# Performance work log

Measured on AMD Instinct MI355X. Metric: run time of the kernel, lower is better.

The kernel has to match this reference:

```python
import jax, jax.numpy as jnp
import numpy as np

M = 64; N_SC = 32; SPS = 8; LENCP = 16; NUMOFDM = 256 // N_SC
BETA = 0.5; SPAN = 16; LENRRC = SPAN * SPS + 1  # 129
FC = 25e6; FS = 10e6 * SPS
CLIP = 1.2; SNR = 10.0; THRES = 8.0
LEN_T = NUMOFDM * (M + LENCP)              # 640
NUMSAMPLES = LEN_T * SPS + LENRRC * 2      # 5378
L1 = LEN_T * SPS + LENRRC - 1              # 5248 (post pulse-shaping length)


def make_rrc():
    # standard root-raised-cosine, unit energy
    t = np.arange(-SPAN * SPS // 2, SPAN * SPS // 2 + 1) / SPS
    h = np.zeros_like(t)
    eps = 1e-9
    t0 = np.abs(t) < eps
    ts = np.abs(np.abs(t) - 1.0 / (4 * BETA)) < eps
    reg = ~(t0 | ts)
    tr = t[reg]
    h[reg] = (np.sin(np.pi * tr * (1 - BETA)) + 4 * BETA * tr * np.cos(np.pi * tr * (1 + BETA))) / (
        np.pi * tr * (1 - (4 * BETA * tr) ** 2))
    h[t0] = 1 + BETA * (4 / np.pi - 1)
    h[ts] = (BETA / np.sqrt(2)) * ((1 + 2 / np.pi) * np.sin(np.pi / (4 * BETA)) +
                                   (1 - 2 / np.pi) * np.cos(np.pi / (4 * BETA)))
    h = h / np.sqrt(np.sum(h ** 2))
    return h.astype(np.float32)


def _conv_full(u, k):
    # torch F.conv1d(x, k.flip(), padding=K-1) == full convolution with k
    K = k.shape[0]
    return jax.lax.conv_general_dilated(
        u[:, None, :], k[::-1][None, None, :], (1,), [(K - 1, K - 1)],
        dimension_numbers=('NCH', 'OIH', 'NCH'))[:, 0, :]


def _pulse_filter(c, rrc):
    return _conv_full(c.real, rrc) + 1j * _conv_full(c.imag, rrc)


def _power_norm(z):
    m = jnp.mean(z, axis=1, keepdims=True)
    s = jnp.std(z, axis=1, ddof=1, keepdims=True)  # torch.std is unbiased
    return (z - m) / (s + 1e-8)


def _forward(x, W_enc, b_enc, W_dec, b_dec, rrc, awgn, startloc):
    B = x.shape[0]
    # --- encoder (linear proxy for ResNetTx) -> 512 reals ---
    z = x.reshape(B, -1) @ W_enc + b_enc
    z = _power_norm(z)
    c = z.reshape(B, 256, 2)
    c = (c[..., 0] + 1j * c[..., 1]).reshape(B, NUMOFDM, N_SC)  # complex64
    # --- DFT precoding ---
    c = jnp.fft.fftshift(jnp.fft.fft(c, axis=-1, norm='ortho'), axes=-1)
    # --- subcarrier mapping (contiguous block, mapping==1) ---
    loc = jnp.arange(startloc, startloc + N_SC)
    data_f = jnp.zeros((B, NUMOFDM, M), jnp.complex64).at[:, :, loc].set(c)
    data_t = jnp.fft.ifft(data_f, axis=-1, norm='ortho')
    data_t = jnp.concatenate([data_t[:, :, -LENCP:], data_t], axis=-1)  # CP
    data_t = data_t.reshape(B, LEN_T)
    # --- zero-stuffed upsampling + RRC pulse shaping ---
    over = jnp.zeros((B, LEN_T * SPS), jnp.complex64).at[:, ::SPS].set(data_t)
    xc = _pulse_filter(over, rrc)  # (B, L1)
    # --- carrier mixing ---
    n = jnp.arange(NUMSAMPLES, dtype=jnp.float32)
    cos_c = jnp.sqrt(2.0) * jnp.cos(2 * jnp.pi * FC * n / FS)
    sin_c = jnp.sqrt(2.0) * jnp.sin(2 * jnp.pi * FC * n / FS)
    data_x = xc.real * cos_c[:L1] - xc.imag * sin_c[:L1]
    # --- clipping ---
    thr = CLIP * jnp.sqrt(jnp.mean(jnp.square(data_x), axis=1, keepdims=True))
    over_amp = jax.nn.relu(jnp.abs(data_x) - thr)
    data_x = (1.0 - over_amp / (jnp.abs(data_x) + 1e-8)) * data_x
    # --- PAPR ---
    tstart = (LENRRC + 1) // 2
    p = jnp.square(data_x[:, tstart:tstart + LEN_T * SPS])
    PAPRdB = 10.0 * jnp.log10(jnp.max(p, axis=1) / jnp.mean(p, axis=1))
    PAPRloss = jnp.mean(jax.nn.relu(PAPRdB - THRES))
    # --- AWGN channel (no fading) ---
    data_r = data_x + awgn
    # --- downconversion + matched filter ---
    rc = data_r * cos_c[:L1] - 1j * (data_r * sin_c[:L1])
    filt = _pulse_filter(rc, rrc)  # (B, L1 + LENRRC - 1) = (B, 5376)
    y = filt[:, LENRRC - 1:filt.shape[1] - LENRRC:SPS]  # (B, LEN_T)
    y = y.reshape(B, NUMOFDM, M + LENCP)[:, :, LENCP:]
    y = jnp.fft.fft(y, axis=-1, norm='ortho')[:, :, loc]
    y = jnp.fft.ifft(jnp.fft.fftshift(y, axes=-1), axis=-1, norm='ortho')
    y = y.reshape(B, NUMOFDM * N_SC)
    y = jnp.stack([y.real, y.imag], axis=-1).reshape(B, 8, 8, 8)
    # --- decoder (linear proxy for ResNetRx) ---
    out = (y.reshape(B, 512) @ W_dec + b_dec).reshape(B, 3, 32, 32)
    return out, PAPRdB, PAPRloss


def setup_inputs() -> dict:
    key = jax.random.key(0)
    ks = jax.random.split(key, 4)
    B = 1024
    x = jax.random.normal(ks[0], (B, 3, 32, 32), jnp.float32)
    W_enc = jax.random.normal(ks[1], (3072, 512), jnp.float32) * 0.02
    b_enc = jnp.zeros((512,), jnp.float32)
    W_dec = jax.random.normal(ks[2], (512, 3072), jnp.float32) * 0.05
    b_dec = jnp.zeros((3072,), jnp.float32)
    rrc = jnp.asarray(make_rrc())
    noise_std = 10.0 ** (-SNR / 20.0)
    awgn = jax.random.normal(ks[3], (B, L1), jnp.float32) * noise_std
    return {"x": x, "W_enc": W_enc, "b_enc": b_enc, "W_dec": W_dec,
            "b_dec": b_dec, "rrc": rrc, "awgn": awgn, "startloc": 7}


def reference(x, W_enc, b_enc, W_dec, b_dec, rrc, awgn, startloc):
    return _forward(x, W_enc, b_enc, W_dec, b_dec, rrc, awgn, startloc)
```

## Files before the change

kernel.cpp:

```cpp
#include <hip/hip_runtime.h>
#include <hip/hip_bf16.h>
#include <math.h>

#define L1_     5248
#define LENRRC_ 129
#define TSTART_ 65
#define NWIN_   5120
#define SWZ(m) ((m) + ((m) >> 3))

typedef __attribute__((ext_vector_type(8))) short s16x8;
typedef __attribute__((ext_vector_type(4))) float f32x4;

__device__ inline ushort bf16_rne(float x) {
    unsigned xb = __float_as_uint(x);
    return (ushort)((xb + 0x7fffu + ((xb >> 16) & 1u)) >> 16);
}

__device__ inline float wave_sum(float v) {
    #pragma unroll
    for (int m = 32; m > 0; m >>= 1) v += __shfl_xor(v, m, 64);
    return v;
}
__device__ inline float wave_max(float v) {
    #pragma unroll
    for (int m = 32; m > 0; m >>= 1) v = fmaxf(v, __shfl_xor(v, m, 64));
    return v;
}

__device__ inline void gl_lds16(const void* g, void* l) {
    __builtin_amdgcn_global_load_lds(
        (const __attribute__((address_space(1))) unsigned int*)g,
        (__attribute__((address_space(3))) unsigned int*)l, 16, 0, 0);
}

__global__ __launch_bounds__(256) void pack_k(const float* __restrict__ W1,
        const float* __restrict__ W2, const float* __restrict__ benc,
        ushort* __restrict__ w1t, ushort* __restrict__ w2t, float* __restrict__ z)
{
    __shared__ ushort tile[64][70];
    const int blk = blockIdx.x, tid = threadIdx.x;
    if (blk < 768) {
        const float* W; ushort* T; int K, N, n0, k0;
        if (blk < 384) {
            int idx = blk;
            W = W1; T = w1t; K = 3072; N = 512;
            n0 = (idx & 7) * 64; k0 = (idx >> 3) * 64;
        } else {
            int idx = blk - 384;
            W = W2; T = w2t; K = 512; N = 3072;
            n0 = (idx % 48) * 64; k0 = (idx / 48) * 64;
        }
        const int cr = tid >> 4, cc = (tid & 15) * 4;
        #pragma unroll
        for (int i = 0; i < 4; ++i) {
            int kk = i * 16 + cr;
            float4 v = *(const float4*)&W[(size_t)(k0 + kk) * N + n0 + cc];
            tile[kk][cc]     = bf16_rne(v.x);
            tile[kk][cc + 1] = bf16_rne(v.y);
            tile[kk][cc + 2] = bf16_rne(v.z);
            tile[kk][cc + 3] = bf16_rne(v.w);
        }
        __syncthreads();
        #pragma unroll
        for (int i = 0; i < 4; ++i) {
            int nn = i * 16 + cr;
            ushort4 h;
            h.x = tile[cc][nn]; h.y = tile[cc + 1][nn];
            h.z = tile[cc + 2][nn]; h.w = tile[cc + 3][nn];
            *(ushort4*)&T[(size_t)(n0 + nn) * K + k0 + cc] = h;
        }
    } else {
        int i = (blk - 768) * 256 + tid;
        z[i] = benc[i & 511];
    }
}

__global__ __launch_bounds__(256) void gemm1_k(const float* __restrict__ Ax,
        const ushort* __restrict__ Bb, float* __restrict__ C, int M, int N, int K,
        int partial)
{
    __shared__ __attribute__((aligned(16))) ushort Asl[64 * 64];
    __shared__ __attribute__((aligned(16))) ushort Bsl[128 * 64];
    const int tid = threadIdx.x;
    const int lane = tid & 63, wave = tid >> 6;
    const int wm = (wave >> 1) * 32, wn = (wave & 1) * 64;
    const int m0 = blockIdx.y * 64, n0 = blockIdx.x * 128;
    const int kch = K / 8, kbeg = blockIdx.z * kch, kend = kbeg + kch;
    const int fm = lane & 15, q = lane >> 4;
    f32x4 acc[2][4] = {};

    int arow[2], akb[2], brow[4], bkb[4];
    #pragma unroll
    for (int j = 0; j < 2; ++j) {
        int c = ((wave * 2 + j) << 6) + lane;
        arow[j] = c >> 3; akb[j] = (c & 7) ^ (arow[j] & 7);
    }
    #pragma unroll
    for (int j = 0; j < 4; ++j) {
        int c = ((wave * 4 + j) << 6) + lane;
        brow[j] = c >> 3; bkb[j] = (c & 7) ^ (brow[j] & 7);
    }

    for (int kt = kbeg; kt < kend; kt += 64) {
        #pragma unroll
        for (int j = 0; j < 4; ++j)
            gl_lds16(&Bb[(size_t)(n0 + brow[j]) * K + kt + bkb[j] * 8],
                     &Bsl[(wave * 4 + j) << 9]);
        #pragma unroll
        for (int j = 0; j < 2; ++j) {
            int c = ((wave * 2 + j) << 6) + lane;
            const float* src = &Ax[(size_t)(m0 + arow[j]) * K + kt + akb[j] * 8];
            float4 v0 = *(const float4*)src;
            float4 v1 = *(const float4*)(src + 4);
            s16x8 hv;
            hv[0] = (short)bf16_rne(v0.x); hv[1] = (short)bf16_rne(v0.y);
            hv[2] = (short)bf16_rne(v0.z); hv[3] = (short)bf16_rne(v0.w);
            hv[4] = (short)bf16_rne(v1.x); hv[5] = (short)bf16_rne(v1.y);
            hv[6] = (short)bf16_rne(v1.z); hv[7] = (short)bf16_rne(v1.w);
            *(s16x8*)&Asl[c * 8] = hv;
        }
        __syncthreads();
        #pragma unroll
        for (int ks = 0; ks < 2; ++ks) {
            s16x8 a[2], b[4];
            #pragma unroll
            for (int mf = 0; mf < 2; ++mf) {
                int r = wm + mf * 16 + fm;
                a[mf] = *(const s16x8*)&Asl[(r << 6) + ((((ks << 2) + q) ^ (r & 7)) << 3)];
            }
            #pragma unroll
            for (int nf = 0; nf < 4; ++nf) {
                int r = wn + nf * 16 + fm;
                b[nf] = *(const s16x8*)&Bsl[(r << 6) + ((((ks << 2) + q) ^ (r & 7)) << 3)];
            }
            #pragma unroll
            for (int mf = 0; mf < 2; ++mf)
                #pragma unroll
                for (int nf = 0; nf < 4; ++nf)
                    acc[mf][nf] = __builtin_amdgcn_mfma_f32_16x16x32_bf16(a[mf], b[nf], acc[mf][nf], 0, 0, 0);
        }
        __syncthreads();
    }

    if (partial) {
        float* Cs = C + (size_t)blockIdx.z * ((size_t)M * N);
        #pragma unroll
        for (int mf = 0; mf < 2; ++mf)
            #pragma unroll
            for (int nf = 0; nf < 4; ++nf)
                #pragma unroll
                for (int r = 0; r < 4; ++r) {
                    int m = m0 + wm + mf * 16 + q * 4 + r;
                    int n = n0 + wn + nf * 16 + fm;
                    Cs[(size_t)m * N + n] = acc[mf][nf][r];
                }
    } else {
        #pragma unroll
        for (int mf = 0; mf < 2; ++mf)
            #pragma unroll
            for (int nf = 0; nf < 4; ++nf)
                #pragma unroll
                for (int r = 0; r < 4; ++r) {
                    int m = m0 + wm + mf * 16 + q * 4 + r;
                    int n = n0 + wn + nf * 16 + fm;
                    atomicAdd(&C[(size_t)m * N + n], acc[mf][nf][r]);
                }
    }
}

__global__ __launch_bounds__(256) void gemm2_k(const ushort* __restrict__ Ab,
        const ushort* __restrict__ Bb, const float* __restrict__ bias,
        const float* __restrict__ papr, float* __restrict__ C,
        float* __restrict__ out_loss, int M, int N, int K)
{
    __shared__ __attribute__((aligned(16))) ushort Asl[64 * 64];
    __shared__ __attribute__((aligned(16))) ushort Bsl[64 * 64];
    __shared__ float red[4];
    const int tid = threadIdx.x;
    const int lane = tid & 63, wave = tid >> 6;
    const int wm = (wave >> 1) * 32, wn = (wave & 1) * 32;
    const int m0 = blockIdx.y * 64, n0 = blockIdx.x * 64;
    const int fm = lane & 15, q = lane >> 4;
    f32x4 acc[2][2] = {};

    int srow[2], skb[2];
    #pragma unroll
    for (int j = 0; j < 2; ++j) {
        int c = ((wave * 2 + j) << 6) + lane;
        srow[j] = c >> 3; skb[j] = (c & 7) ^ (srow[j] & 7);
    }

    for (int kt = 0; kt < K; kt += 64) {
        #pragma unroll
        for (int j = 0; j < 2; ++j) {
            gl_lds16(&Ab[(size_t)(m0 + srow[j]) * K + kt + skb[j] * 8],
                     &Asl[(wave * 2 + j) << 9]);
            gl_lds16(&Bb[(size_t)(n0 + srow[j]) * K + kt + skb[j] * 8],
                     &Bsl[(wave * 2 + j) << 9]);
        }
        __syncthreads();
        #pragma unroll
        for (int ks = 0; ks < 2; ++ks) {
            s16x8 a[2], b[2];
            #pragma unroll
            for (int mf = 0; mf < 2; ++mf) {
                int r = wm + mf * 16 + fm;
                a[mf] = *(const s16x8*)&Asl[(r << 6) + ((((ks << 2) + q) ^ (r & 7)) << 3)];
            }
            #pragma unroll
            for (int nf = 0; nf < 2; ++nf) {
                int r = wn + nf * 16 + fm;
                b[nf] = *(const s16x8*)&Bsl[(r << 6) + ((((ks << 2) + q) ^ (r & 7)) << 3)];
            }
            #pragma unroll
            for (int mf = 0; mf < 2; ++mf)
                #pragma unroll
                for (int nf = 0; nf < 2; ++nf)
                    acc[mf][nf] = __builtin_amdgcn_mfma_f32_16x16x32_bf16(a[mf], b[nf], acc[mf][nf], 0, 0, 0);
        }
        __syncthreads();
    }

    #pragma unroll
    for (int mf = 0; mf < 2; ++mf)
        #pragma unroll
        for (int nf = 0; nf < 2; ++nf)
            #pragma unroll
            for (int r = 0; r < 4; ++r) {
                int m = m0 + wm + mf * 16 + q * 4 + r;
                int n = n0 + wn + nf * 16 + fm;
                C[(size_t)m * N + n] = acc[mf][nf][r] + bias[n];
            }

    if (blockIdx.x == 0 && blockIdx.y == 0) {
        float s = 0.f;
        for (int i = tid; i < 1024; i += 256) { float v = papr[i] - 8.f; s += v > 0.f ? v : 0.f; }
        s = wave_sum(s);
        if (lane == 0) red[wave] = s;
        __syncthreads();
        if (tid == 0) *out_loss = (red[0] + red[1] + red[2] + red[3]) * (1.f / 1024.f);
    }
}

__global__ __launch_bounds__(512, 4) void mega_k(const float* __restrict__ z,
        const float* __restrict__ benc,
        const float* __restrict__ rrc, const float* __restrict__ awgn,
        const int* __restrict__ slocp, ushort* __restrict__ y5b,
        float* __restrict__ papr, float* __restrict__ out_papr, int nsp)
{
    __shared__ float  zl[2][512];
    __shared__ float2 trti[2][672];
    __shared__ float  hl[132];
    __shared__ float  csl[16], ssl[16];
    __shared__ float2 cs64[64];
    __shared__ float  ct[64];
    __shared__ __attribute__((aligned(16))) float2 gcs[130];
    __shared__ float  dxr[2][SWZ(L1_ - 1) + 1];
    __shared__ float  red[2][8], red2[2][8];

    const int b0 = blockIdx.x * 2, b1 = b0 + 1;
    const int tid = threadIdx.x;
    const int lane = tid & 63, wv = tid >> 6;
    const int sloc = *slocp;
    const float S2048 = 0.02209708691207961f;

    if (tid < 64) {
        float ang = 0.09817477042468103f * (float)tid;
        float s, c; sincosf(ang, &s, &c);
        cs64[tid] = make_float2(c, s);
    }
    if (tid >= 64 && tid < 80) {
        int t = tid - 64;
        float ang = 1.9634954084936207f * (float)t;
        float s, c; sincosf(ang, &s, &c);
        csl[t] = 1.4142135623730951f * c; ssl[t] = 1.4142135623730951f * s;
    }
    if (tid >= 96 && tid < 160) {
        int t = (tid - 96) & 31, row = (tid - 96) >> 5;
        int idx = (t < 16) ? t : (640 + t);
        trti[row][idx] = make_float2(0.f, 0.f);
    }
    if (tid >= 160 && tid < 224) {
        int j = tid - 160;
        float v = 0.f;
        if (j & 1) { float s, c; sincosf(0.04908738521234052f * (float)j, &s, &c); v = c / s; }
        ct[j] = v;
    }
    if (tid >= 256 && tid < 256 + LENRRC_) hl[tid - 256] = rrc[tid - 256];

    float va, vb;
    if (nsp) {
        va = benc[tid]; vb = va;
        const float* zp0 = z + (size_t)b0 * 512;
        const float* zp1 = z + (size_t)b1 * 512;
        for (int s = 0; s < nsp; ++s) {
            va += zp0[(size_t)s * 524288 + tid];
            vb += zp1[(size_t)s * 524288 + tid];
        }
    } else {
        va = z[(size_t)b0 * 512 + tid];
        vb = z[(size_t)b1 * 512 + tid];
    }
    __syncthreads();

    if (tid < LENRRC_) {
        int neg = (16 - (tid & 15)) & 15;
        gcs[tid] = make_float2(hl[tid] * csl[neg], hl[tid] * ssl[neg]);
    }

    {
        float S0 = wave_sum(va), Q0 = wave_sum(va * va);
        float S1 = wave_sum(vb), Q1 = wave_sum(vb * vb);
        if (lane == 0) { red[0][wv] = S0; red2[0][wv] = Q0; red[1][wv] = S1; red2[1][wv] = Q1; }
    }
    __syncthreads();
    {
        float S0 = 0.f, Q0 = 0.f, S1 = 0.f, Q1 = 0.f;
        #pragma unroll
        for (int w = 0; w < 8; ++w) {
            S0 += red[0][w]; Q0 += red2[0][w];
            S1 += red[1][w]; Q1 += red2[1][w];
        }
        float m0 = S0 * (1.f / 512.f), m1 = S1 * (1.f / 512.f);
        float i0 = 1.f / (sqrtf((Q0 - S0 * m0) * (1.f / 511.f)) + 1e-8f);
        float i1 = 1.f / (sqrtf((Q1 - S1 * m1) * (1.f / 511.f)) + 1e-8f);
        float sg = ((tid >> 1) & 1) ? -1.f : 1.f;
        zl[0][tid] = (va - m0) * i0 * sg;
        zl[1][tid] = (vb - m1) * i1 * sg;
    }
    __syncthreads();

    {
        int r = tid >> 8, t = tid & 255;
        int s = t >> 5, j = t & 31;
        int base = s * 80;
        const float2* zs = (const float2*)&zl[r][s * 64];
        int n = 2 * j + 1;
        float Zr = 0.f, Zi = 0.f, Tr = 0.f, Ti = 0.f;
        #pragma unroll 4
        for (int q = 0; q < 32; ++q) {
            float2 a = zs[q];
            float w = ct[(n - 2 * q) & 63];
            Zr += a.x; Zi += a.y;
            Tr += a.x * w; Ti += a.y * w;
        }
        {
            float2 cw = cs64[(n * sloc) & 63];
            float Ar = Zr - Ti, Ai = Zi + Tr;
            float dr = S2048 * (Ar * cw.x - Ai * cw.y);
            float di = S2048 * (Ai * cw.x + Ar * cw.y);
            trti[r][base + 32 + n] = make_float2(dr, di);
            if (n >= 48) trti[r][base + n - 32] = make_float2(dr, di);
        }
        {
            int n2 = 2 * j;
            float2 a = zs[j];
            float2 cw = cs64[(n2 * sloc) & 63];
            const float RS2 = 0.7071067811865476f;
            float dr = RS2 * (a.x * cw.x - a.y * cw.y);
            float di = RS2 * (a.y * cw.x + a.x * cw.y);
            trti[r][base + 32 + n2] = make_float2(dr, di);
            if (n2 >= 48) trti[r][base + n2 - 32] = make_float2(dr, di);
        }
    }
    __syncthreads();

    float ss0 = 0.f, ss1 = 0.f;
    for (int tsk = tid; tsk < 1312; tsk += 512) {
        int a = tsk >> 1, g = tsk & 1;
        float ar0[4] = {}, ai0[4] = {}, ar1[4] = {}, ai1[4] = {};
        #pragma unroll 4
        for (int d = 0; d < 16; ++d) {
            float2 t0 = trti[0][16 + a - d];
            float2 t1 = trti[1][16 + a - d];
            #pragma unroll
            for (int r = 0; r < 4; ++r) {
                float h = hl[g * 4 + r + 8 * d];
                ar0[r] += t0.x * h; ai0[r] += t0.y * h;
                ar1[r] += t1.x * h; ai1[r] += t1.y * h;
            }
        }
        if (g == 0) {
            float2 t0 = trti[0][a], t1 = trti[1][a];
            float h = hl[128];
            ar0[0] += t0.x * h; ai0[0] += t0.y * h;
            ar1[0] += t1.x * h; ai1[0] += t1.y * h;
        }
        int cb = (a & 1) * 8;
        #pragma unroll
        for (int r = 0; r < 4; ++r) {
            int rr = g * 4 + r;
            float cv = csl[cb + rr], sv = ssl[cb + rr];
            float v0 = ar0[r] * cv - ai0[r] * sv;
            float v1 = ar1[r] * cv - ai1[r] * sv;
            dxr[0][SWZ(a * 8 + rr)] = v0;
            dxr[1][SWZ(a * 8 + rr)] = v1;
            ss0 += v0 * v0; ss1 += v1 * v1;
        }
    }
    ss0 = wave_sum(ss0); ss1 = wave_sum(ss1);
    if (lane == 0) { red[0][wv] = ss0; red[1][wv] = ss1; }
    __syncthreads();
    float thr0, thr1;
    {
        float S0 = 0.f, S1 = 0.f;
        #pragma unroll
        for (int w = 0; w < 8; ++w) { S0 += red[0][w]; S1 += red[1][w]; }
        thr0 = 1.2f * sqrtf(S0 / (float)L1_);
        thr1 = 1.2f * sqrtf(S1 / (float)L1_);
    }
    __syncthreads();

    float pm0 = 0.f, ps0 = 0.f, pm1 = 0.f, ps1 = 0.f;
    {
        const float4* ag0 = (const float4*)&awgn[(size_t)b0 * L1_];
        const float4* ag1 = (const float4*)&awgn[(size_t)b1 * L1_];
        for (int ii = tid; ii < 1312; ii += 512) {
            float4 a0 = ag0[ii], a1 = ag1[ii];
            int i = ii * 4;
            #pragma unroll
            for (int e = 0; e < 4; ++e) {
                int idx = i + e;
                bool win = (idx >= TSTART_ && idx < TSTART_ + NWIN_);
                float aw0 = (e == 0) ? a0.x : (e == 1) ? a0.y : (e == 2) ? a0.z : a0.w;
                float aw1 = (e == 0) ? a1.x : (e == 1) ? a1.y : (e == 2) ? a1.z : a1.w;
                {
                    float x = dxr[0][SWZ(idx)];
                    float ax = fabsf(x);
                    float over = fmaxf(ax - thr0, 0.f);
                    float y = (1.f - over / (ax + 1e-8f)) * x;
                    if (win) { float p = y * y; ps0 += p; pm0 = fmaxf(pm0, p); }
                    dxr[0][SWZ(idx)] = y + aw0;
                }
                {
                    float x = dxr[1][SWZ(idx)];
                    float ax = fabsf(x);
                    float over = fmaxf(ax - thr1, 0.f);
                    float y = (1.f - over / (ax + 1e-8f)) * x;
                    if (win) { float p = y * y; ps1 += p; pm1 = fmaxf(pm1, p); }
                    dxr[1][SWZ(idx)] = y + aw1;
                }
            }
        }
    }
    ps0 = wave_sum(ps0); pm0 = wave_max(pm0);
    ps1 = wave_sum(ps1); pm1 = wave_max(pm1);
    if (lane == 0) { red[0][wv] = ps0; red2[0][wv] = pm0; red[1][wv] = ps1; red2[1][wv] = pm1; }
    __syncthreads();
    if (tid == 0) {
        float s0 = 0.f, m0 = 0.f, s1 = 0.f, m1 = 0.f;
        #pragma unroll
        for (int w = 0; w < 8; ++w) {
            s0 += red[0][w]; m0 = fmaxf(m0, red2[0][w]);
            s1 += red[1][w]; m1 = fmaxf(m1, red2[1][w]);
        }
        float p0 = 10.f * log10f(m0 / (s0 / (float)NWIN_));
        float p1 = 10.f * log10f(m1 / (s1 / (float)NWIN_));
        papr[b0] = p0; out_papr[b0] = p0;
        papr[b1] = p1; out_papr[b1] = p1;
    }
    __syncthreads();

    {
        int s = wv, n = lane;
        int T0 = s * 80 + n + 32;
        int base = 9 * T0;
        float ar0 = 0.f, ai0 = 0.f, ar1 = 0.f, ai1 = 0.f;
        int db = 0;
        #pragma unroll 4
        for (int e = 0; e < 16; ++e) {
            float4 g01 = *(const float4*)&gcs[db];
            float4 g23 = *(const float4*)&gcs[db + 2];
            float4 g45 = *(const float4*)&gcs[db + 4];
            float4 g67 = *(const float4*)&gcs[db + 6];
            float gx[8] = { g01.x, g01.z, g23.x, g23.z, g45.x, g45.z, g67.x, g67.z };
            float gy[8] = { g01.y, g01.w, g23.y, g23.w, g45.y, g45.w, g67.y, g67.w };
            #pragma unroll
            for (int u = 0; u < 8; ++u) {
                int off = (u == 0) ? 0 : (u + 1);
                float v0 = dxr[0][base - off];
                float v1 = dxr[1][base - off];
                ar0 += v0 * gx[u]; ai0 += v0 * gy[u];
                ar1 += v1 * gx[u]; ai1 += v1 * gy[u];
            }
            base -= 9; db += 8;
        }
        {
            float2 g = gcs[128];
            float v0 = dxr[0][base], v1 = dxr[1][base];
            ar0 += v0 * g.x; ai0 += v0 * g.y;
            ar1 += v1 * g.x; ai1 += v1 * g.y;
        }
        bool odd = (n & 1);
        float wr0 = odd ? -ar0 : ar0, wi0 = odd ? ai0 : -ai0;
        float wr1 = odd ? -ar1 : ar1, wi1 = odd ? ai1 : -ai1;
        float2 cw = cs64[(n * sloc) & 63];
        trti[0][s * 64 + n] = make_float2(wr0 * cw.x + wi0 * cw.y, wi0 * cw.x - wr0 * cw.y);
        trti[1][s * 64 + n] = make_float2(wr1 * cw.x + wi1 * cw.y, wi1 * cw.x - wr1 * cw.y);
    }
    __syncthreads();

    {
        int r = tid >> 8, t = tid & 255;
        int s = t >> 5, q = t & 31;
        const float2* wt = &trti[r][s * 64];
        float Wr = 0.f, Wi = 0.f, Ur = 0.f, Ui = 0.f;
        #pragma unroll 4
        for (int u = 0; u < 32; ++u) {
            float2 a = wt[2 * u + 1];
            float w = ct[(2 * q - 2 * u - 1) & 63];
            Wr += a.x; Wi += a.y;
            Ur += a.x * w; Ui += a.y * w;
        }
        float2 e = wt[2 * q];
        float sgn = (q & 1) ? -S2048 : S2048;
        float yr = sgn * (32.f * e.x + Wr - Ui);
        float yi = sgn * (32.f * e.y + Wi + Ur);
        ushort2 h; h.x = bf16_rne(yr); h.y = bf16_rne(yi);
        *(ushort2*)&y5b[(size_t)(b0 + r) * 512 + (s * 32 + q) * 2] = h;
    }
}

extern "C" void kernel_launch(void* const* d_in, const int* in_sizes, int n_in,
                              void* d_out, int out_size, void* d_ws, size_t ws_size,
                              hipStream_t stream) {
    const float* x    = (const float*)d_in[0];
    const float* Wenc = (const float*)d_in[1];
    const float* benc = (const float*)d_in[2];
    const float* Wdec = (const float*)d_in[3];
    const float* bdec = (const float*)d_in[4];
    const float* rrc  = (const float*)d_in[5];
    const float* awgn = (const float*)d_in[6];
    const int* sloc   = (const int*)d_in[7];
    float* out = (float*)d_out;

    char* wsb = (char*)d_ws;
    ushort* w1t  = (ushort*)wsb;                     wsb += (size_t)512 * 3072 * 2;
    ushort* w2t  = (ushort*)wsb;                     wsb += (size_t)3072 * 512 * 2;
    ushort* y5b  = (ushort*)wsb;                     wsb += (size_t)1024 * 512 * 2;
    float*  papr = (float*)wsb;                      wsb += 1024 * 4;
    float*  zbuf = (float*)wsb;
    size_t head = (size_t)((char*)zbuf - (char*)d_ws);
    int partial = (ws_size >= head + (size_t)8 * 1024 * 512 * 4) ? 1 : 0;

    float* out_papr = out + (size_t)1024 * 3072;
    float* out_loss = out_papr + 1024;

    pack_k<<<partial ? 768 : 2816, 256, 0, stream>>>(Wenc, Wdec, benc, w1t, w2t, zbuf);
    gemm1_k<<<dim3(4, 16, 8), 256, 0, stream>>>(x, w1t, zbuf, 1024, 512, 3072, partial);
    mega_k<<<512, 512, 0, stream>>>(zbuf, benc, rrc, awgn, sloc, y5b, papr, out_papr,
                                    partial ? 8 : 0);
    gemm2_k<<<dim3(48, 16, 1), 256, 0, stream>>>(y5b, w2t, bdec, papr, out, out_loss, 1024, 3072, 512);
}
```

Measured before the change: 145.2 us.

## Double mega_k block size to 1024 threads and split per-row work

Launches the fused OFDM kernel with 1024 threads per block instead of 512. Normalization, the final receive filter and the DFT stages now give each thread one batch row, or half of a DFT sum combined with a lane shuffle, instead of two rows or the full sum. The goal is more in-flight threads and shorter per-thread dependency chains on a latency-bound kernel. The costs are heavier register pressure under the 1024-thread launch bound, idle threads in loops that only cover 1312 tasks, and extra shuffles and barrier cost.

After: 153.8 us. +6.0%, slower.

```diff
diff --git a/kernel.cpp b/kernel.cpp
--- a/kernel.cpp
+++ b/kernel.cpp
@@ -242,7 +242,7 @@
     }
 }
 
-__global__ __launch_bounds__(512, 4) void mega_k(const float* __restrict__ z,
+__global__ __launch_bounds__(1024, 4) void mega_k(const float* __restrict__ z,
         const float* __restrict__ benc,
         const float* __restrict__ rrc, const float* __restrict__ awgn,
         const int* __restrict__ slocp, ushort* __restrict__ y5b,
@@ -256,7 +256,7 @@
     __shared__ float  ct[64];
     __shared__ __attribute__((aligned(16))) float2 gcs[130];
     __shared__ float  dxr[2][SWZ(L1_ - 1) + 1];
-    __shared__ float  red[2][8], red2[2][8];
+    __shared__ float  red[2][16], red2[2][16];
 
     const int b0 = blockIdx.x * 2, b1 = b0 + 1;
     const int tid = threadIdx.x;
@@ -288,18 +288,15 @@
     }
     if (tid >= 256 && tid < 256 + LENRRC_) hl[tid - 256] = rrc[tid - 256];
 
-    float va, vb;
+    const int zrow = tid >> 9, zi = tid & 511;
+    float va;
     if (nsp) {
-        va = benc[tid]; vb = va;
-        const float* zp0 = z + (size_t)b0 * 512;
-        const float* zp1 = z + (size_t)b1 * 512;
-        for (int s = 0; s < nsp; ++s) {
-            va += zp0[(size_t)s * 524288 + tid];
-            vb += zp1[(size_t)s * 524288 + tid];
-        }
+        va = benc[zi];
+        const float* zp = z + (size_t)(b0 + zrow) * 512;
+        for (int s = 0; s < nsp; ++s)
+            va += zp[(size_t)s * 524288 + zi];
     } else {
-        va = z[(size_t)b0 * 512 + tid];
-        vb = z[(size_t)b1 * 512 + tid];
+        va = z[(size_t)(b0 + zrow) * 512 + zi];
     }
     __syncthreads();
 
@@ -309,64 +306,67 @@
     }
 
     {
-        float S0 = wave_sum(va), Q0 = wave_sum(va * va);
-        float S1 = wave_sum(vb), Q1 = wave_sum(vb * vb);
-        if (lane == 0) { red[0][wv] = S0; red2[0][wv] = Q0; red[1][wv] = S1; red2[1][wv] = Q1; }
-    }
-    __syncthreads();
-    {
-        float S0 = 0.f, Q0 = 0.f, S1 = 0.f, Q1 = 0.f;
-        #pragma unroll
-        for (int w = 0; w < 8; ++w) {
-            S0 += red[0][w]; Q0 += red2[0][w];
-            S1 += red[1][w]; Q1 += red2[1][w];
-        }
-        float m0 = S0 * (1.f / 512.f), m1 = S1 * (1.f / 512.f);
-        float i0 = 1.f / (sqrtf((Q0 - S0 * m0) * (1.f / 511.f)) + 1e-8f);
-        float i1 = 1.f / (sqrtf((Q1 - S1 * m1) * (1.f / 511.f)) + 1e-8f);
-        float sg = ((tid >> 1) & 1) ? -1.f : 1.f;
-        zl[0][tid] = (va - m0) * i0 * sg;
-        zl[1][tid] = (vb - m1) * i1 * sg;
-    }
-    __syncthreads();
-
-    {
-        int r = tid >> 8, t = tid & 255;
+        float S = wave_sum(va);
+        float Q = wave_sum(va * va);
+        if (lane == 0) { red[0][wv] = S; red2[0][wv] = Q; }
+    }
+    __syncthreads();
+    {
+        int rb = zrow * 8;
+        float S = 0.f, Q = 0.f;
+        #pragma unroll
+        for (int w = 0; w < 8; ++w) { S += red[0][rb + w]; Q += red2[0][rb + w]; }
+        float mean = S * (1.f / 512.f);
+        float var = (Q - S * mean) * (1.f / 511.f);
+        float inv = 1.f / (sqrtf(var) + 1e-8f);
+        float sg = ((zi >> 1) & 1) ? -1.f : 1.f;
+        zl[zrow][zi] = (va - mean) * inv * sg;
+    }
+    __syncthreads();
+
+    {
+        int slot = tid >> 1, h = tid & 1;
+        int r = slot >> 8, t = slot & 255;
         int s = t >> 5, j = t & 31;
         int base = s * 80;
         const float2* zs = (const float2*)&zl[r][s * 64];
         int n = 2 * j + 1;
         float Zr = 0.f, Zi = 0.f, Tr = 0.f, Ti = 0.f;
+        int qb = 16 * h;
         #pragma unroll 4
-        for (int q = 0; q < 32; ++q) {
+        for (int q = qb; q < qb + 16; ++q) {
             float2 a = zs[q];
             float w = ct[(n - 2 * q) & 63];
             Zr += a.x; Zi += a.y;
             Tr += a.x * w; Ti += a.y * w;
         }
-        {
-            float2 cw = cs64[(n * sloc) & 63];
-            float Ar = Zr - Ti, Ai = Zi + Tr;
-            float dr = S2048 * (Ar * cw.x - Ai * cw.y);
-            float di = S2048 * (Ai * cw.x + Ar * cw.y);
-            trti[r][base + 32 + n] = make_float2(dr, di);
-            if (n >= 48) trti[r][base + n - 32] = make_float2(dr, di);
-        }
-        {
-            int n2 = 2 * j;
-            float2 a = zs[j];
-            float2 cw = cs64[(n2 * sloc) & 63];
-            const float RS2 = 0.7071067811865476f;
-            float dr = RS2 * (a.x * cw.x - a.y * cw.y);
-            float di = RS2 * (a.y * cw.x + a.x * cw.y);
-            trti[r][base + 32 + n2] = make_float2(dr, di);
-            if (n2 >= 48) trti[r][base + n2 - 32] = make_float2(dr, di);
+        Zr += __shfl_xor(Zr, 1, 64); Zi += __shfl_xor(Zi, 1, 64);
+        Tr += __shfl_xor(Tr, 1, 64); Ti += __shfl_xor(Ti, 1, 64);
+        if (h == 0) {
+            {
+                float2 cw = cs64[(n * sloc) & 63];
+                float Ar = Zr - Ti, Ai = Zi + Tr;
+                float dr = S2048 * (Ar * cw.x - Ai * cw.y);
+                float di = S2048 * (Ai * cw.x + Ar * cw.y);
+                trti[r][base + 32 + n] = make_float2(dr, di);
+                if (n >= 48) trti[r][base + n - 32] = make_float2(dr, di);
+            }
+            {
+                int n2 = 2 * j;
+                float2 a = zs[j];
+                float2 cw = cs64[(n2 * sloc) & 63];
+                const float RS2 = 0.7071067811865476f;
+                float dr = RS2 * (a.x * cw.x - a.y * cw.y);
+                float di = RS2 * (a.y * cw.x + a.x * cw.y);
+                trti[r][base + 32 + n2] = make_float2(dr, di);
+                if (n2 >= 48) trti[r][base + n2 - 32] = make_float2(dr, di);
+            }
         }
     }
     __syncthreads();
 
     float ss0 = 0.f, ss1 = 0.f;
-    for (int tsk = tid; tsk < 1312; tsk += 512) {
+    for (int tsk = tid; tsk < 1312; tsk += 1024) {
         int a = tsk >> 1, g = tsk & 1;
         float ar0[4] = {}, ai0[4] = {}, ar1[4] = {}, ai1[4] = {};
         #pragma unroll 4
@@ -405,7 +405,7 @@
     {
         float S0 = 0.f, S1 = 0.f;
         #pragma unroll
-        for (int w = 0; w < 8; ++w) { S0 += red[0][w]; S1 += red[1][w]; }
+        for (int w = 0; w < 16; ++w) { S0 += red[0][w]; S1 += red[1][w]; }
         thr0 = 1.2f * sqrtf(S0 / (float)L1_);
         thr1 = 1.2f * sqrtf(S1 / (float)L1_);
     }
@@ -415,7 +415,7 @@
     {
         const float4* ag0 = (const float4*)&awgn[(size_t)b0 * L1_];
         const float4* ag1 = (const float4*)&awgn[(size_t)b1 * L1_];
-        for (int ii = tid; ii < 1312; ii += 512) {
+        for (int ii = tid; ii < 1312; ii += 1024) {
             float4 a0 = ag0[ii], a1 = ag1[ii];
             int i = ii * 4;
             #pragma unroll
@@ -450,7 +450,7 @@
     if (tid == 0) {
         float s0 = 0.f, m0 = 0.f, s1 = 0.f, m1 = 0.f;
         #pragma unroll
-        for (int w = 0; w < 8; ++w) {
+        for (int w = 0; w < 16; ++w) {
             s0 += red[0][w]; m0 = fmaxf(m0, red2[0][w]);
             s1 += red[1][w]; m1 = fmaxf(m1, red2[1][w]);
         }
@@ -462,10 +462,11 @@
     __syncthreads();
 
     {
-        int s = wv, n = lane;
+        int r = tid >> 9, o = tid & 511;
+        int s = o >> 6, n = o & 63;
         int T0 = s * 80 + n + 32;
         int base = 9 * T0;
-        float ar0 = 0.f, ai0 = 0.f, ar1 = 0.f, ai1 = 0.f;
+        float ar = 0.f, ai = 0.f;
         int db = 0;
         #pragma unroll 4
         for (int e = 0; e < 16; ++e) {
@@ -478,46 +479,47 @@
             #pragma unroll
             for (int u = 0; u < 8; ++u) {
                 int off = (u == 0) ? 0 : (u + 1);
-                float v0 = dxr[0][base - off];
-                float v1 = dxr[1][base - off];
-                ar0 += v0 * gx[u]; ai0 += v0 * gy[u];
-                ar1 += v1 * gx[u]; ai1 += v1 * gy[u];
+                float v = dxr[r][base - off];
+                ar += v * gx[u]; ai += v * gy[u];
             }
             base -= 9; db += 8;
         }
         {
             float2 g = gcs[128];
-            float v0 = dxr[0][base], v1 = dxr[1][base];
-            ar0 += v0 * g.x; ai0 += v0 * g.y;
-            ar1 += v1 * g.x; ai1 += v1 * g.y;
+            float v = dxr[r][base];
+            ar += v * g.x; ai += v * g.y;
         }
         bool odd = (n & 1);
-        float wr0 = odd ? -ar0 : ar0, wi0 = odd ? ai0 : -ai0;
-        float wr1 = odd ? -ar1 : ar1, wi1 = odd ? ai1 : -ai1;
+        float wr = odd ? -ar : ar, wi = odd ? ai : -ai;
         float2 cw = cs64[(n * sloc) & 63];
-        trti[0][s * 64 + n] = make_float2(wr0 * cw.x + wi0 * cw.y, wi0 * cw.x - wr0 * cw.y);
-        trti[1][s * 64 + n] = make_float2(wr1 * cw.x + wi1 * cw.y, wi1 * cw.x - wr1 * cw.y);
-    }
-    __syncthreads();
-
-    {
-        int r = tid >> 8, t = tid & 255;
+        trti[r][s * 64 + n] = make_float2(wr * cw.x + wi * cw.y, wi * cw.x - wr * cw.y);
+    }
+    __syncthreads();
+
+    {
+        int slot = tid >> 1, h = tid & 1;
+        int r = slot >> 8, t = slot & 255;
         int s = t >> 5, q = t & 31;
         const float2* wt = &trti[r][s * 64];
         float Wr = 0.f, Wi = 0.f, Ur = 0.f, Ui = 0.f;
+        int ub = 16 * h;
         #pragma unroll 4
-        for (int u = 0; u < 32; ++u) {
+        for (int u = ub; u < ub + 16; ++u) {
             float2 a = wt[2 * u + 1];
             float w = ct[(2 * q - 2 * u - 1) & 63];
             Wr += a.x; Wi += a.y;
             Ur += a.x * w; Ui += a.y * w;
         }
-        float2 e = wt[2 * q];
-        float sgn = (q & 1) ? -S2048 : S2048;
-        float yr = sgn * (32.f * e.x + Wr - Ui);
-        float yi = sgn * (32.f * e.y + Wi + Ur);
-        ushort2 h; h.x = bf16_rne(yr); h.y = bf16_rne(yi);
-        *(ushort2*)&y5b[(size_t)(b0 + r) * 512 + (s * 32 + q) * 2] = h;
+        Wr += __shfl_xor(Wr, 1, 64); Wi += __shfl_xor(Wi, 1, 64);
+        Ur += __shfl_xor(Ur, 1, 64); Ui += __shfl_xor(Ui, 1, 64);
+        if (h == 0) {
+            float2 e = wt[2 * q];
+            float sgn = (q & 1) ? -S2048 : S2048;
+            float yr = sgn * (32.f * e.x + Wr - Ui);
+            float yi = sgn * (32.f * e.y + Wi + Ur);
+            ushort2 hv; hv.x = bf16_rne(yr); hv.y = bf16_rne(yi);
+            *(ushort2*)&y5b[(size_t)(b0 + r) * 512 + (s * 32 + q) * 2] = hv;
+        }
     }
 }
 
@@ -548,7 +550,7 @@
 
     pack_k<<<partial ? 768 : 2816, 256, 0, stream>>>(Wenc, Wdec, benc, w1t, w2t, zbuf);
     gemm1_k<<<dim3(4, 16, 8), 256, 0, stream>>>(x, w1t, zbuf, 1024, 512, 3072, partial);
-    mega_k<<<512, 512, 0, stream>>>(zbuf, benc, rrc, awgn, sloc, y5b, papr, out_papr,
-                                    partial ? 8 : 0);
+    mega_k<<<512, 1024, 0, stream>>>(zbuf, benc, rrc, awgn, sloc, y5b, papr, out_papr,
+                                     partial ? 8 : 0);
     gemm2_k<<<dim3(48, 16, 1), 256, 0, stream>>>(y5b, w2t, bdec, papr, out, out_loss, 1024, 3072, 512);
 }
```
